# Kernel optimization log

Measured on AMD Instinct MI355X. Metric: run time of the kernel, lower is better.

Reference implementation:

```python
import jax, jax.numpy as jnp
import numpy as np

B, D, H, W = 32, 256, 32, 32
K = 1024
COMMITMENT_COST = 0.25


def setup_inputs() -> dict:
    key = jax.random.key(0)
    k1, k2 = jax.random.split(key)
    z = jax.random.normal(k1, (B, D, H, W), dtype=jnp.float32)
    # torch init: uniform_(-1/K, 1/K)
    emb_weight = jax.random.uniform(k2, (K, D), dtype=jnp.float32,
                                    minval=-1.0 / K, maxval=1.0 / K)
    return {"z": z, "emb_weight": emb_weight}


def reference(z, emb_weight):
    b, c, h, w = z.shape
    # [B, D, H, W] -> [B*H*W, D]
    z_flat = jnp.transpose(z, (0, 2, 3, 1)).reshape(-1, c)
    # squared-distance: ||z||^2 + ||e||^2 - 2 z.e  -> [N, K]
    distances = (jnp.sum(z_flat ** 2, axis=1, keepdims=True)
                 + jnp.sum(emb_weight ** 2, axis=1)[None, :]
                 - 2.0 * jnp.matmul(z_flat, emb_weight.T))
    encoding_indices = jnp.argmin(distances, axis=1)  # [N]
    z_q = emb_weight[encoding_indices]                # [N, D]
    z_q = z_q.reshape(b, h, w, c).transpose(0, 3, 1, 2)  # [B, D, H, W]

    q_latent_loss = jnp.mean((jax.lax.stop_gradient(z_q) - z) ** 2)
    e_latent_loss = jnp.mean((z_q - jax.lax.stop_gradient(z)) ** 2)
    loss = q_latent_loss + COMMITMENT_COST * e_latent_loss

    # straight-through estimator
    z_q = z + jax.lax.stop_gradient(z_q - z)
    return z_q, loss, encoding_indices
```

## Files before the change

kernel.cpp:

```cpp
#include <hip/hip_runtime.h>

#define NPTS  32768
#define DIM   256

#define ZQ_OFF   0
#define LOSS_OFF 8388608
#define IDX_OFF  8388609

typedef __attribute__((ext_vector_type(8))) short short8;
typedef __attribute__((ext_vector_type(4))) float f32x4;
typedef unsigned short ushort_t;
typedef unsigned int u32;

__device__ __forceinline__ int z_base(int n) { return ((n >> 10) << 18) | (n & 1023); }

__device__ __forceinline__ ushort_t f2bf(float f) {
    u32 u = __float_as_uint(f);
    u += 0x7FFFu + ((u >> 16) & 1u);
    return (ushort_t)(u >> 16);
}

__device__ __forceinline__ unsigned long long pack_vi(float v, int i) {
    u32 u = __float_as_uint(v);
    u32 key = (u & 0x80000000u) ? ~u : u;
    return ((unsigned long long)key << 32) | (u32)i;
}

__device__ __forceinline__ float np_half_sq(const float* __restrict__ p, int stride) {
    float S[16];
#pragma unroll
    for (int l = 0; l < 16; ++l) {
        float t[8];
#pragma unroll
        for (int j = 0; j < 8; ++j) {
            float v = p[(j * 16 + l) * stride];
            t[j] = __fmul_rn(v, v);
        }
        S[l] = __fadd_rn(__fadd_rn(__fadd_rn(t[0], t[1]), __fadd_rn(t[2], t[3])),
                         __fadd_rn(__fadd_rn(t[4], t[5]), __fadd_rn(t[6], t[7])));
    }
    float u[8];
#pragma unroll
    for (int i = 0; i < 8; ++i) u[i] = __fadd_rn(S[i], S[i + 8]);
    float v4[4];
#pragma unroll
    for (int i = 0; i < 4; ++i) v4[i] = __fadd_rn(u[i], u[i + 4]);
    return __fadd_rn(__fadd_rn(v4[0], v4[2]), __fadd_rn(v4[1], v4[3]));
}
__device__ __forceinline__ float np_sum256_sq(const float* __restrict__ p, int stride) {
    return __fadd_rn(np_half_sq(p, stride), np_half_sq(p + 128 * stride, stride));
}

__device__ __forceinline__ float np_half_sq_abs(const float* __restrict__ p, int stride, float* aacc) {
    float S[16]; float a = *aacc;
#pragma unroll
    for (int l = 0; l < 16; ++l) {
        float t[8];
#pragma unroll
        for (int j = 0; j < 8; ++j) {
            float v = p[(j * 16 + l) * stride];
            t[j] = __fmul_rn(v, v);
            a = __fadd_rn(a, fabsf(v));
        }
        S[l] = __fadd_rn(__fadd_rn(__fadd_rn(t[0], t[1]), __fadd_rn(t[2], t[3])),
                         __fadd_rn(__fadd_rn(t[4], t[5]), __fadd_rn(t[6], t[7])));
    }
    float u[8];
#pragma unroll
    for (int i = 0; i < 8; ++i) u[i] = __fadd_rn(S[i], S[i + 8]);
    float v4[4];
#pragma unroll
    for (int i = 0; i < 4; ++i) v4[i] = __fadd_rn(u[i], u[i + 4]);
    *aacc = a;
    return __fadd_rn(__fadd_rn(v4[0], v4[2]), __fadd_rn(v4[1], v4[3]));
}

__global__ __launch_bounds__(256) void setup_kernel(
    const float* __restrict__ z, const float* __restrict__ emb,
    float* __restrict__ z2, float* __restrict__ eps,
    float* __restrict__ e2, float* __restrict__ e2h,
    ushort_t* __restrict__ ebf,
    double* __restrict__ loss_acc, unsigned int* __restrict__ ticket)
{
    if (blockIdx.x < 128) {
        int n = blockIdx.x * 256 + threadIdx.x;
        const float* p = z + z_base(n);
        float a = 0.0f;
        float h0 = np_half_sq_abs(p, 1024, &a);
        float h1 = np_half_sq_abs(p + 128 * 1024, 1024, &a);
        z2[n] = __fadd_rn(h0, h1);
        eps[n] = __builtin_fmaf(1e-5f, a, 3e-4f);
        if (blockIdx.x == 0 && threadIdx.x == 0) { *loss_acc = 0.0; *ticket = 0u; }
    } else {
        int kb = (blockIdx.x - 128) * 256;
        for (int i = threadIdx.x; i < 8192; i += 256) {
            int klocal = i >> 5, c16 = i & 31;
            int k = kb + klocal;
            int r = k & 31, ktc = k >> 5;
            int dslot = c16 ^ (r & 7);
            const float* e = emb + k * 256 + dslot * 8;
            short8 ov;
#pragma unroll
            for (int j = 0; j < 8; ++j) ov[j] = (short)f2bf(e[j]);
            *(short8*)(ebf + ktc * 8192 + r * 256 + c16 * 8) = ov;
        }
        int k = kb + threadIdx.x;
        float s = np_sum256_sq(emb + k * DIM, 1);
        e2[k] = s;
        e2h[k] = 0.5f * s;
    }
}

#define ZS_STRIDE 264

__device__ __forceinline__ void async_cp16(const ushort_t* g, ushort_t* l) {
    __builtin_amdgcn_global_load_lds(
        (const __attribute__((address_space(1))) u32*)g,
        (__attribute__((address_space(3))) u32*)l, 16, 0, 0);
}

__global__ __launch_bounds__(256, 3) void dist_kernel(
    const float* __restrict__ z, const float* __restrict__ emb,
    const ushort_t* __restrict__ ebf,
    const float* __restrict__ z2w, const float* __restrict__ e2w,
    const float* __restrict__ e2hw, const float* __restrict__ epsw,
    float* __restrict__ out_idx)
{
    __shared__ __align__(16) short uni[16896];
    __shared__ __align__(16) int cl[2048];
    __shared__ float e2hS[1024];
    __shared__ float epsS[64], z2S[64];
    __shared__ unsigned int cntS[64];
    __shared__ unsigned long long bestS[64];
    __shared__ int ovfS;

    const int tid = threadIdx.x;
    const int w  = tid >> 6;
    const int l  = tid & 63;
    const int lq = l >> 4;
    const int lr = l & 15;
    const int n0 = blockIdx.x << 6;
    const int zb = z_base(n0);
    const int pbase = w << 4;

    if (tid < 64) {
        cntS[tid] = 0u; bestS[tid] = 0x7FFFFFFFFFFFFFFFULL;
        epsS[tid] = epsw[n0 + tid]; z2S[tid] = z2w[n0 + tid];
    }
    if (tid == 0) ovfS = 0;
    for (int i = tid; i < 1024; i += 256) e2hS[i] = e2hw[i];

    {
        short* zs = uni;
        int q = tid & 15, d0 = tid >> 4;
#pragma unroll 4
        for (int i = 0; i < 16; ++i) {
            int d = d0 + 16 * i;
            float4 v = *(const float4*)(z + zb + (d << 10) + 4 * q);
            zs[(4 * q + 0) * ZS_STRIDE + d] = (short)f2bf(v.x);
            zs[(4 * q + 1) * ZS_STRIDE + d] = (short)f2bf(v.y);
            zs[(4 * q + 2) * ZS_STRIDE + d] = (short)f2bf(v.z);
            zs[(4 * q + 3) * ZS_STRIDE + d] = (short)f2bf(v.w);
        }
    }
    __syncthreads();

    short8 af[8];
#pragma unroll
    for (int d8 = 0; d8 < 8; ++d8)
        af[d8] = *(const short8*)(uni + (pbase + lr) * ZS_STRIDE + d8 * 32 + lq * 8);

    float eps_r[4], Mr[4];
#pragma unroll
    for (int r = 0; r < 4; ++r) {
        eps_r[r] = epsS[pbase + lq * 4 + r];
        Mr[r] = -3.4e38f;
    }
    __syncthreads();

    {
        const ushort_t* gs = ebf + w * 2048 + (l << 3);
        ushort_t* ld = (ushort_t*)uni + w * 2048;
        async_cp16(gs,        ld);
        async_cp16(gs +  512, ld +  512);
        async_cp16(gs + 1024, ld + 1024);
        async_cp16(gs + 1536, ld + 1536);
    }

    f32x4 acc[2];
#pragma unroll
    for (int nt = 0; nt < 2; ++nt) {
        float e = e2hS[16 * nt + lr];
        f32x4 iv = { -e, -e, -e, -e };
        acc[nt] = iv;
    }
    __syncthreads();

    const int c16base = (lq << 3) ^ ((lr & 7) << 3);

#pragma unroll 1
    for (int kt = 0; kt < 32; ++kt) {
        if (kt < 31) {
            const ushort_t* gs = ebf + (kt + 1) * 8192 + w * 2048 + (l << 3);
            ushort_t* ld = (ushort_t*)uni + (((kt + 1) & 1) << 13) + w * 2048;
            async_cp16(gs,        ld);
            async_cp16(gs +  512, ld +  512);
            async_cp16(gs + 1024, ld + 1024);
            async_cp16(gs + 1536, ld + 1536);
        }
        const short* esb = uni + ((kt & 1) << 13);
#pragma unroll
        for (int dt = 0; dt < 8; ++dt) {
            const int c16s = (((dt << 2) + lq) ^ (lr & 7)) << 3;
            short8 b0 = *(const short8*)(esb + (lr)      * 256 + c16s);
            short8 b1 = *(const short8*)(esb + (16 + lr) * 256 + c16s);
            acc[0] = __builtin_amdgcn_mfma_f32_16x16x32_bf16(af[dt], b0, acc[0], 0, 0, 0);
            acc[1] = __builtin_amdgcn_mfma_f32_16x16x32_bf16(af[dt], b1, acc[1], 0, 0, 0);
        }
        {
            float mx[4];
#pragma unroll
            for (int r = 0; r < 4; ++r) mx[r] = fmaxf(acc[0][r], acc[1][r]);
#pragma unroll
            for (int s = 1; s <= 8; s <<= 1)
#pragma unroll
                for (int r = 0; r < 4; ++r)
                    mx[r] = fmaxf(mx[r], __shfl_xor(mx[r], s, 64));
            float thr[4];
#pragma unroll
            for (int r = 0; r < 4; ++r) {
                Mr[r] = fmaxf(Mr[r], mx[r]);
                thr[r] = Mr[r] - eps_r[r];
            }
#pragma unroll
            for (int nt = 0; nt < 2; ++nt)
#pragma unroll
                for (int r = 0; r < 4; ++r) {
                    if (acc[nt][r] >= thr[r]) {
                        int p = pbase + lq * 4 + r;
                        int kk = kt * 32 + 16 * nt + lr;
                        unsigned int pos = atomicAdd(&cntS[p], 1u);
                        if (pos < 32u) cl[p * 32 + pos] = kk;
                        else atomicMax(&ovfS, 1);
                    }
                }
        }
        if (kt < 31) {
#pragma unroll
            for (int nt = 0; nt < 2; ++nt) {
                float e = e2hS[(kt + 1) * 32 + 16 * nt + lr];
                f32x4 iv = { -e, -e, -e, -e };
                acc[nt] = iv;
            }
        }
        __syncthreads();
    }

    float* zx = (float*)uni;
    const int pt = tid & 63;
    const int s0 = tid >> 6;
    unsigned int nc = cntS[pt]; if (nc > 32u) nc = 32u;
    bool  act[8]; int kE[8]; float accE[8];
#pragma unroll
    for (int j = 0; j < 8; ++j) {
        unsigned int s = (unsigned int)s0 + 4u * j;
        act[j] = s < nc;
        kE[j] = act[j] ? cl[pt * 32 + s] : 0;
        accE[j] = 0.0f;
    }
#pragma unroll 1
    for (int dt = 0; dt < 8; ++dt) {
        const int dbase = dt * 32;
        __syncthreads();
        {
            int q = tid & 15, dd0 = tid >> 4;
            float4 v0 = *(const float4*)(z + zb + ((dbase + dd0) << 10) + 4 * q);
            float4 v1 = *(const float4*)(z + zb + ((dbase + dd0 + 16) << 10) + 4 * q);
            *(float4*)(zx + dd0 * 68 + 4 * q) = v0;
            *(float4*)(zx + (dd0 + 16) * 68 + 4 * q) = v1;
        }
        __syncthreads();
#pragma unroll
        for (int j = 0; j < 8; ++j) {
            if (!act[j]) continue;
            const float* er = emb + kE[j] * 256 + dbase;
            float ev[32];
#pragma unroll
            for (int c = 0; c < 8; ++c) *(float4*)(ev + 4 * c) = *(const float4*)(er + 4 * c);
            float a = accE[j];
#pragma unroll
            for (int dd = 0; dd < 32; ++dd)
                a = __builtin_fmaf(zx[dd * 68 + pt], ev[dd], a);
            accE[j] = a;
        }
    }
#pragma unroll
    for (int j = 0; j < 8; ++j) {
        if (!act[j]) continue;
        int k = kE[j];
        float t1 = __fadd_rn(z2S[pt], e2w[k]);
        float d  = __fsub_rn(t1, __fmul_rn(2.0f, accE[j]));
        atomicMin(&bestS[pt], pack_vi(d, k));
    }
    __syncthreads();

    if (ovfS) {
        for (int row = 0; row < 64; ++row) {
            if (cntS[row] <= 32u) continue;
            float fa[4] = {0.f, 0.f, 0.f, 0.f};
            for (int dt = 0; dt < 8; ++dt) {
                const int dbase = dt * 32;
                __syncthreads();
                {
                    int q = tid & 15, dd0 = tid >> 4;
                    float4 v0 = *(const float4*)(z + zb + ((dbase + dd0) << 10) + 4 * q);
                    float4 v1 = *(const float4*)(z + zb + ((dbase + dd0 + 16) << 10) + 4 * q);
                    *(float4*)(zx + dd0 * 68 + 4 * q) = v0;
                    *(float4*)(zx + (dd0 + 16) * 68 + 4 * q) = v1;
                }
                __syncthreads();
                for (int c = 0; c < 4; ++c) {
                    const float* er = emb + (tid + 256 * c) * 256 + dbase;
                    for (int dd = 0; dd < 32; ++dd)
                        fa[c] = __builtin_fmaf(zx[dd * 68 + row], er[dd], fa[c]);
                }
            }
            for (int c = 0; c < 4; ++c) {
                int k = tid + 256 * c;
                float t1 = __fadd_rn(z2S[row], e2w[k]);
                float d  = __fsub_rn(t1, __fmul_rn(2.0f, fa[c]));
                atomicMin(&bestS[row], pack_vi(d, k));
            }
            __syncthreads();
        }
    }

    if (tid < 64)
        out_idx[n0 + tid] = (float)(unsigned int)(bestS[tid] & 0xFFFFFFFFULL);
}

__global__ __launch_bounds__(256) void zq_loss_kernel(
    const float* __restrict__ z, const float* __restrict__ emb,
    const float* __restrict__ idxv, float* __restrict__ zq,
    double* __restrict__ loss_acc, unsigned int* __restrict__ ticket,
    float* __restrict__ out_loss)
{
    const int tl = threadIdx.x & 127;
    const int h  = threadIdx.x >> 7;
    const int n  = blockIdx.x * 128 + tl;
    const int kk = (int)idxv[n];
    const float* er = emb + kk * DIM + (h << 7);
    const int zb2 = z_base(n) + (h << 17);
    double s = 0.0;
#pragma unroll 8
    for (int dd = 0; dd < 128; ++dd) {
        float ev = er[dd];
        float zv = z[zb2 + (dd << 10)];
        zq[zb2 + (dd << 10)] = ev;
        float df = ev - zv;
        s = fma((double)df, (double)df, s);
    }
    for (int off = 32; off; off >>= 1) s += __shfl_down(s, off, 64);
    __shared__ double sred[4];
    if ((threadIdx.x & 63) == 0) sred[threadIdx.x >> 6] = s;
    __syncthreads();
    if (threadIdx.x == 0) {
        atomicAdd(loss_acc, (sred[0] + sred[1]) + (sred[2] + sred[3]));
        __threadfence();
        unsigned int old = atomicAdd(ticket, 1u);
        if (old == gridDim.x - 1) {
            double total = atomicAdd(loss_acc, 0.0);
            out_loss[0] = (float)(1.25 * (total / 8388608.0));
        }
    }
}

extern "C" void kernel_launch(void* const* d_in, const int* in_sizes, int n_in,
                              void* d_out, int out_size, void* d_ws, size_t ws_size,
                              hipStream_t stream) {
    const float* z   = (const float*)d_in[0];
    const float* emb = (const float*)d_in[1];
    float* out = (float*)d_out;

    float* z2w = (float*)d_ws;
    float* epsw = (float*)((char*)d_ws + 131072);
    float* e2w = (float*)((char*)d_ws + 262144);
    float* e2hw = (float*)((char*)d_ws + 266240);
    ushort_t* ebf = (ushort_t*)((char*)d_ws + 270336);
    double* loss_acc = (double*)((char*)d_ws + 794624);
    unsigned int* ticket = (unsigned int*)((char*)d_ws + 794632);

    setup_kernel<<<132, 256, 0, stream>>>(z, emb, z2w, epsw, e2w, e2hw, ebf,
                                          loss_acc, ticket);
    dist_kernel<<<NPTS / 64, 256, 0, stream>>>(z, emb, ebf, z2w, e2w, e2hw, epsw,
                                               out + IDX_OFF);
    zq_loss_kernel<<<256, 256, 0, stream>>>(z, emb, out + IDX_OFF,
                                            out + ZQ_OFF, loss_acc, ticket,
                                            out + LOSS_OFF);
}
```

Before: 232.7 us.

## Split codebook across four blocks per point tile with global atomic argmin

The distance kernel now splits the 1024-entry codebook into four quarters, launching four blocks per 64-point tile, each scanning 8 codebook tiles instead of 32. Per-point best (distance, index) pairs are merged through 64-bit atomicMin in a global workspace array, which setup initialises, and the zq/loss kernel decodes the index and writes it out. The goal is more parallelism and occupancy (launch bounds raised to 4, smaller LDS arrays). The cost is that each z tile is loaded and converted to bf16 four times, plus extra global atomics. The per-quarter candidate list is now capped at 16, so the fp32 overflow fallback may trigger more often. Setup and zq_loss grids are also reshaped to use more blocks.

```diff
diff --git a/kernel.cpp b/kernel.cpp
--- a/kernel.cpp
+++ b/kernel.cpp
@@ -11,6 +11,7 @@
 typedef __attribute__((ext_vector_type(4))) float f32x4;
 typedef unsigned short ushort_t;
 typedef unsigned int u32;
+typedef unsigned long long u64;
 
 __device__ __forceinline__ int z_base(int n) { return ((n >> 10) << 18) | (n & 1023); }
 
@@ -20,10 +21,10 @@
     return (ushort_t)(u >> 16);
 }
 
-__device__ __forceinline__ unsigned long long pack_vi(float v, int i) {
+__device__ __forceinline__ u64 pack_vi(float v, int i) {
     u32 u = __float_as_uint(v);
     u32 key = (u & 0x80000000u) ? ~u : u;
-    return ((unsigned long long)key << 32) | (u32)i;
+    return ((u64)key << 32) | (u32)i;
 }
 
 __device__ __forceinline__ float np_half_sq(const float* __restrict__ p, int stride) {
@@ -79,7 +80,7 @@
     const float* __restrict__ z, const float* __restrict__ emb,
     float* __restrict__ z2, float* __restrict__ eps,
     float* __restrict__ e2, float* __restrict__ e2h,
-    ushort_t* __restrict__ ebf,
+    ushort_t* __restrict__ ebf, u64* __restrict__ bestG,
     double* __restrict__ loss_acc, unsigned int* __restrict__ ticket)
 {
     if (blockIdx.x < 128) {
@@ -90,10 +91,11 @@
         float h1 = np_half_sq_abs(p + 128 * 1024, 1024, &a);
         z2[n] = __fadd_rn(h0, h1);
         eps[n] = __builtin_fmaf(1e-5f, a, 3e-4f);
+        bestG[n] = 0x7FFFFFFFFFFFFFFFULL;
         if (blockIdx.x == 0 && threadIdx.x == 0) { *loss_acc = 0.0; *ticket = 0u; }
     } else {
-        int kb = (blockIdx.x - 128) * 256;
-        for (int i = threadIdx.x; i < 8192; i += 256) {
+        int kb = (blockIdx.x - 128) * 64;
+        for (int i = threadIdx.x; i < 2048; i += 256) {
             int klocal = i >> 5, c16 = i & 31;
             int k = kb + klocal;
             int r = k & 31, ktc = k >> 5;
@@ -104,10 +106,12 @@
             for (int j = 0; j < 8; ++j) ov[j] = (short)f2bf(e[j]);
             *(short8*)(ebf + ktc * 8192 + r * 256 + c16 * 8) = ov;
         }
-        int k = kb + threadIdx.x;
-        float s = np_sum256_sq(emb + k * DIM, 1);
-        e2[k] = s;
-        e2h[k] = 0.5f * s;
+        if (threadIdx.x < 64) {
+            int k = kb + threadIdx.x;
+            float s = np_sum256_sq(emb + k * DIM, 1);
+            e2[k] = s;
+            e2h[k] = 0.5f * s;
+        }
     }
 }
 
@@ -119,19 +123,18 @@
         (__attribute__((address_space(3))) u32*)l, 16, 0, 0);
 }
 
-__global__ __launch_bounds__(256, 3) void dist_kernel(
+__global__ __launch_bounds__(256, 4) void dist_kernel(
     const float* __restrict__ z, const float* __restrict__ emb,
     const ushort_t* __restrict__ ebf,
     const float* __restrict__ z2w, const float* __restrict__ e2w,
     const float* __restrict__ e2hw, const float* __restrict__ epsw,
-    float* __restrict__ out_idx)
+    u64* __restrict__ bestG)
 {
     __shared__ __align__(16) short uni[16896];
-    __shared__ __align__(16) int cl[2048];
-    __shared__ float e2hS[1024];
+    __shared__ __align__(16) int cl[1024];
+    __shared__ float e2hS[256];
     __shared__ float epsS[64], z2S[64];
     __shared__ unsigned int cntS[64];
-    __shared__ unsigned long long bestS[64];
     __shared__ int ovfS;
 
     const int tid = threadIdx.x;
@@ -139,16 +142,18 @@
     const int l  = tid & 63;
     const int lq = l >> 4;
     const int lr = l & 15;
-    const int n0 = blockIdx.x << 6;
+    const int kq = blockIdx.x & 3;
+    const int n0 = (blockIdx.x >> 2) << 6;
     const int zb = z_base(n0);
     const int pbase = w << 4;
+    const int ktg0 = kq << 3;
 
     if (tid < 64) {
-        cntS[tid] = 0u; bestS[tid] = 0x7FFFFFFFFFFFFFFFULL;
+        cntS[tid] = 0u;
         epsS[tid] = epsw[n0 + tid]; z2S[tid] = z2w[n0 + tid];
     }
     if (tid == 0) ovfS = 0;
-    for (int i = tid; i < 1024; i += 256) e2hS[i] = e2hw[i];
+    e2hS[tid] = e2hw[(kq << 8) + tid];
 
     {
         short* zs = uni;
@@ -179,7 +184,7 @@
     __syncthreads();
 
     {
-        const ushort_t* gs = ebf + w * 2048 + (l << 3);
+        const ushort_t* gs = ebf + ktg0 * 8192 + w * 2048 + (l << 3);
         ushort_t* ld = (ushort_t*)uni + w * 2048;
         async_cp16(gs,        ld);
         async_cp16(gs +  512, ld +  512);
@@ -196,12 +201,10 @@
     }
     __syncthreads();
 
-    const int c16base = (lq << 3) ^ ((lr & 7) << 3);
-
 #pragma unroll 1
-    for (int kt = 0; kt < 32; ++kt) {
-        if (kt < 31) {
-            const ushort_t* gs = ebf + (kt + 1) * 8192 + w * 2048 + (l << 3);
+    for (int kt = 0; kt < 8; ++kt) {
+        if (kt < 7) {
+            const ushort_t* gs = ebf + (ktg0 + kt + 1) * 8192 + w * 2048 + (l << 3);
             ushort_t* ld = (ushort_t*)uni + (((kt + 1) & 1) << 13) + w * 2048;
             async_cp16(gs,        ld);
             async_cp16(gs +  512, ld +  512);
@@ -238,14 +241,14 @@
                 for (int r = 0; r < 4; ++r) {
                     if (acc[nt][r] >= thr[r]) {
                         int p = pbase + lq * 4 + r;
-                        int kk = kt * 32 + 16 * nt + lr;
+                        int kk = ((ktg0 + kt) << 5) + 16 * nt + lr;
                         unsigned int pos = atomicAdd(&cntS[p], 1u);
-                        if (pos < 32u) cl[p * 32 + pos] = kk;
+                        if (pos < 16u) cl[p * 16 + pos] = kk;
                         else atomicMax(&ovfS, 1);
                     }
                 }
         }
-        if (kt < 31) {
+        if (kt < 7) {
 #pragma unroll
             for (int nt = 0; nt < 2; ++nt) {
                 float e = e2hS[(kt + 1) * 32 + 16 * nt + lr];
@@ -259,13 +262,13 @@
     float* zx = (float*)uni;
     const int pt = tid & 63;
     const int s0 = tid >> 6;
-    unsigned int nc = cntS[pt]; if (nc > 32u) nc = 32u;
-    bool  act[8]; int kE[8]; float accE[8];
-#pragma unroll
-    for (int j = 0; j < 8; ++j) {
+    unsigned int nc = cntS[pt]; if (nc > 16u) nc = 16u;
+    bool  act[4]; int kE[4]; float accE[4];
+#pragma unroll
+    for (int j = 0; j < 4; ++j) {
         unsigned int s = (unsigned int)s0 + 4u * j;
         act[j] = s < nc;
-        kE[j] = act[j] ? cl[pt * 32 + s] : 0;
+        kE[j] = act[j] ? cl[pt * 16 + s] : 0;
         accE[j] = 0.0f;
     }
 #pragma unroll 1
@@ -281,7 +284,7 @@
         }
         __syncthreads();
 #pragma unroll
-        for (int j = 0; j < 8; ++j) {
+        for (int j = 0; j < 4; ++j) {
             if (!act[j]) continue;
             const float* er = emb + kE[j] * 256 + dbase;
             float ev[32];
@@ -295,19 +298,19 @@
         }
     }
 #pragma unroll
-    for (int j = 0; j < 8; ++j) {
+    for (int j = 0; j < 4; ++j) {
         if (!act[j]) continue;
         int k = kE[j];
         float t1 = __fadd_rn(z2S[pt], e2w[k]);
         float d  = __fsub_rn(t1, __fmul_rn(2.0f, accE[j]));
-        atomicMin(&bestS[pt], pack_vi(d, k));
+        atomicMin(&bestG[n0 + pt], pack_vi(d, k));
     }
     __syncthreads();
 
     if (ovfS) {
         for (int row = 0; row < 64; ++row) {
-            if (cntS[row] <= 32u) continue;
-            float fa[4] = {0.f, 0.f, 0.f, 0.f};
+            if (cntS[row] <= 16u) continue;
+            float fa = 0.0f;
             for (int dt = 0; dt < 8; ++dt) {
                 const int dbase = dt * 32;
                 __syncthreads();
@@ -319,41 +322,35 @@
                     *(float4*)(zx + (dd0 + 16) * 68 + 4 * q) = v1;
                 }
                 __syncthreads();
-                for (int c = 0; c < 4; ++c) {
-                    const float* er = emb + (tid + 256 * c) * 256 + dbase;
-                    for (int dd = 0; dd < 32; ++dd)
-                        fa[c] = __builtin_fmaf(zx[dd * 68 + row], er[dd], fa[c]);
-                }
+                const float* er = emb + ((kq << 8) + tid) * 256 + dbase;
+                for (int dd = 0; dd < 32; ++dd)
+                    fa = __builtin_fmaf(zx[dd * 68 + row], er[dd], fa);
             }
-            for (int c = 0; c < 4; ++c) {
-                int k = tid + 256 * c;
-                float t1 = __fadd_rn(z2S[row], e2w[k]);
-                float d  = __fsub_rn(t1, __fmul_rn(2.0f, fa[c]));
-                atomicMin(&bestS[row], pack_vi(d, k));
-            }
+            int k = (kq << 8) + tid;
+            float t1 = __fadd_rn(z2S[row], e2w[k]);
+            float d  = __fsub_rn(t1, __fmul_rn(2.0f, fa));
+            atomicMin(&bestG[n0 + row], pack_vi(d, k));
             __syncthreads();
         }
     }
-
-    if (tid < 64)
-        out_idx[n0 + tid] = (float)(unsigned int)(bestS[tid] & 0xFFFFFFFFULL);
 }
 
 __global__ __launch_bounds__(256) void zq_loss_kernel(
     const float* __restrict__ z, const float* __restrict__ emb,
-    const float* __restrict__ idxv, float* __restrict__ zq,
+    const u64* __restrict__ bestG, float* __restrict__ zq,
     double* __restrict__ loss_acc, unsigned int* __restrict__ ticket,
-    float* __restrict__ out_loss)
+    float* __restrict__ out_loss, float* __restrict__ out_idx)
 {
-    const int tl = threadIdx.x & 127;
-    const int h  = threadIdx.x >> 7;
-    const int n  = blockIdx.x * 128 + tl;
-    const int kk = (int)idxv[n];
-    const float* er = emb + kk * DIM + (h << 7);
-    const int zb2 = z_base(n) + (h << 17);
+    const int tl = threadIdx.x & 63;
+    const int q  = threadIdx.x >> 6;
+    const int n  = blockIdx.x * 64 + tl;
+    const int kk = (int)(u32)(bestG[n] & 0xFFFFFFFFULL);
+    if (q == 0) out_idx[n] = (float)kk;
+    const float* er = emb + kk * DIM + (q << 6);
+    const int zb2 = z_base(n) + (q << 16);
     double s = 0.0;
 #pragma unroll 8
-    for (int dd = 0; dd < 128; ++dd) {
+    for (int dd = 0; dd < 64; ++dd) {
         float ev = er[dd];
         float zv = z[zb2 + (dd << 10)];
         zq[zb2 + (dd << 10)] = ev;
@@ -389,12 +386,13 @@
     ushort_t* ebf = (ushort_t*)((char*)d_ws + 270336);
     double* loss_acc = (double*)((char*)d_ws + 794624);
     unsigned int* ticket = (unsigned int*)((char*)d_ws + 794632);
-
-    setup_kernel<<<132, 256, 0, stream>>>(z, emb, z2w, epsw, e2w, e2hw, ebf,
-                                          loss_acc, ticket);
-    dist_kernel<<<NPTS / 64, 256, 0, stream>>>(z, emb, ebf, z2w, e2w, e2hw, epsw,
-                                               out + IDX_OFF);
-    zq_loss_kernel<<<256, 256, 0, stream>>>(z, emb, out + IDX_OFF,
-                                            out + ZQ_OFF, loss_acc, ticket,
-                                            out + LOSS_OFF);
-}
+    u64* bestG = (u64*)((char*)d_ws + 794640);
+
+    setup_kernel<<<144, 256, 0, stream>>>(z, emb, z2w, epsw, e2w, e2hw, ebf,
+                                          bestG, loss_acc, ticket);
+    dist_kernel<<<(NPTS / 64) * 4, 256, 0, stream>>>(z, emb, ebf, z2w, e2w, e2hw,
+                                                     epsw, bestG);
+    zq_loss_kernel<<<NPTS / 64, 256, 0, stream>>>(z, emb, bestG, out + ZQ_OFF,
+                                                  loss_acc, ticket,
+                                                  out + LOSS_OFF, out + IDX_OFF);
+}
```

New measurement: 287.9 us. 23.7% more time.
